# Optimization experiments

Measured on AMD Instinct MI355X. Metric: run time of the kernel, lower is better.

## Reference

```python
import jax, jax.numpy as jnp
import numpy as np

WIN = (2, 7, 7)
DIL = (1, 2, 2)
SHIFT = (1, 3, 3)
HEADS = 3

def _rel_index(win):
    # relative position index, identical to the torch buffer construction
    cs = np.stack(np.meshgrid(np.arange(win[0]), np.arange(win[1]), np.arange(win[2]), indexing='ij'))
    flat = cs.reshape(3, -1)                                  # (3, N)
    rel = (flat[:, :, None] - flat[:, None, :]).transpose(1, 2, 0)  # (N, N, 3)
    rel[..., 0] += win[0] - 1
    rel[..., 1] += win[1] - 1
    rel[..., 2] += win[2] - 1
    rel[..., 1] *= 2 * win[2] - 1
    rel[..., 0] *= (2 * win[1] - 1) * (2 * win[2] - 1)
    return rel.sum(-1)                                        # (N, N) int

REL_IDX = _rel_index(WIN)

def _partition(x, win, dil):
    # x: (B, S, H, W, C) -> (numWin*B, N, C) with dilated window layout
    B, S, H, W, C = x.shape
    x = x.reshape(B, S // (dil[0] * win[0]), dil[0], win[0],
                  H // (dil[1] * win[1]), dil[1], win[1],
                  W // (dil[2] * win[2]), dil[2], win[2], C)
    x = x.transpose(0, 2, 5, 8, 1, 4, 7, 3, 6, 9, 10)
    return x.reshape(-1, win[0] * win[1] * win[2], C)

def _reverse(wins, win, dil, S, H, W, C):
    B = wins.shape[0] * win[0] * win[1] * win[2] // (S * H * W)
    x = wins.reshape(B, dil[0], dil[1], dil[2],
                     S // (dil[0] * win[0]), H // (dil[1] * win[1]), W // (dil[2] * win[2]),
                     win[0], win[1], win[2], C)
    x = x.transpose(0, 4, 1, 7, 5, 2, 8, 6, 3, 9, 10)
    return x.reshape(B, S, H, W, C)

def setup_inputs() -> dict:
    key = jax.random.key(0)
    ks = jax.random.split(key, 4)
    B, S, H, W, C = 4, 8, 112, 112, 96
    tbl = (2 * WIN[0] - 1) * (2 * WIN[1] - 1) * (2 * WIN[2] - 1)
    return {
        'x': jax.random.normal(ks[0], (B, S * H * W, C), jnp.float32),
        'qkv_w': jax.random.normal(ks[1], (3 * C, C), jnp.float32) * 0.02,
        'qkv_b': jnp.zeros((3 * C,), jnp.float32),
        'proj_w': jax.random.normal(ks[2], (C, C), jnp.float32) * 0.02,
        'proj_b': jnp.zeros((C,), jnp.float32),
        'rel_bias_table': jax.random.normal(ks[3], (tbl, HEADS), jnp.float32) * 0.02,
        'S': 8, 'H': 112, 'W': 112,
    }

def reference(x, qkv_w, qkv_b, proj_w, proj_b, rel_bias_table, S, H, W):
    B, L, C = x.shape
    hd = C // HEADS
    scale = hd ** -0.5
    x = x.reshape(B, S, H, W, C)
    true = tuple(w * d for w, d in zip(WIN, DIL))
    tshift = tuple(s * d for s, d in zip(SHIFT, DIL))
    pad_d = (-S) % true[0]; pad_b = (-H) % true[1]; pad_r = (-W) % true[2]
    x = jnp.pad(x, ((0, 0), (0, pad_d), (0, pad_b), (0, pad_r), (0, 0)))
    Sp, Hp, Wp = S + pad_d, H + pad_b, W + pad_r
    if any(s > 0 for s in SHIFT):
        x = jnp.roll(x, (-tshift[0], -tshift[1], -tshift[2]), axis=(1, 2, 3))
    xw = _partition(x, WIN, DIL)                              # (B_, N, C)
    B_, N, _ = xw.shape
    qkv = (xw @ qkv_w.T + qkv_b).reshape(B_, N, 3, HEADS, hd).transpose(2, 0, 3, 1, 4)
    q, k, v = qkv[0] * scale, qkv[1], qkv[2]                  # (B_, h, N, d)
    attn = jnp.einsum('bhnd,bhmd->bhnm', q, k)
    bias = rel_bias_table[REL_IDX.reshape(-1)].reshape(N, N, HEADS).transpose(2, 0, 1)
    attn = jax.nn.softmax(attn + bias[None], axis=-1)
    out = jnp.einsum('bhnm,bhmd->bhnd', attn, v).transpose(0, 2, 1, 3).reshape(B_, N, C)
    out = out @ proj_w.T + proj_b
    x = _reverse(out, WIN, DIL, Sp, Hp, Wp, C)
    if any(s > 0 for s in SHIFT):
        x = jnp.roll(x, tshift, axis=(1, 2, 3))
    x = x[:, :S, :H, :W, :]
    return x.reshape(B, S * H * W, C)
```

## Files before the change

kernel.cpp:

```cpp
#include <hip/hip_runtime.h>
#include <hip/hip_bf16.h>


typedef __attribute__((ext_vector_type(8))) short short8;
typedef __attribute__((ext_vector_type(4))) float f32x4;

#define WQ_ELEMS (288 * 96)
#define WP_ELEMS (96 * 96)
#define BIAS_ELEMS (3 * 112 * 112)
#define LOG2E 1.4426950408889634f

__device__ __forceinline__ unsigned short f2bf(float f) {
  __hip_bfloat16 h = __float2bfloat16(f);
  return *reinterpret_cast<unsigned short*>(&h);
}

__device__ __forceinline__ unsigned int pack_bf2(float a, float b) {
  unsigned int r;
  asm("v_cvt_pk_bf16_f32 %0, %1, %2" : "=v"(r) : "v"(a), "v"(b));
  return r;
}

__device__ __forceinline__ float exp2_hw(float x) {
  float r;
  asm("v_exp_f32 %0, %1" : "=v"(r) : "v"(x));
  return r;
}

__global__ __launch_bounds__(256) void prep_kernel(
    const float* __restrict__ qkv_w, const float* __restrict__ proj_w,
    const float* __restrict__ tbl, unsigned short* __restrict__ wq,
    unsigned short* __restrict__ wp, float* __restrict__ bias) {
  int i = blockIdx.x * 256 + threadIdx.x;
  if (i < WQ_ELEMS) wq[i] = f2bf(qkv_w[i]);
  if (i < WP_ELEMS) wp[i] = f2bf(proj_w[i]);
  if (i < BIAS_ELEMS) {
    int h = i / 12544; int rem = i - h * 12544;
    int m = rem / 112; int n = rem - m * 112;
    float v = -1e30f;
    if (m < 98 && n < 98) {
      int m0 = m / 49, mr = m - m0 * 49, m1 = mr / 7, m2 = mr - m1 * 7;
      int n0 = n / 49, nr = n - n0 * 49, n1 = nr / 7, n2 = nr - n1 * 7;
      int idx = (m0 - n0 + 1) * 169 + (m1 - n1 + 6) * 13 + (m2 - n2 + 6);
      v = tbl[idx * 3 + h] * LOG2E;
    }
    bias[i] = v;
  }
}


__global__ __launch_bounds__(512, 4) void winattn_kernel(
    const float* __restrict__ x, const float* __restrict__ qkv_b,
    const float* __restrict__ proj_b, const unsigned short* __restrict__ wq,
    const unsigned short* __restrict__ wp, const float* __restrict__ bias,
    float* __restrict__ out) {

  __shared__ __align__(16) unsigned short lds[40512];
  __shared__ int eoff[98];

  unsigned short* Qf  = lds;
  unsigned short* Kf  = lds + 9408;
  unsigned short* Vtf = lds + 18816;
  unsigned short* Xf  = lds + 31104;

  const int tid  = threadIdx.x;
  const int wv   = tid >> 6;
  const int lane = tid & 63;
  const int l    = lane & 15;
  const int q    = lane >> 4;

  const short8 zero8 = {0, 0, 0, 0, 0, 0, 0, 0};

  int t1 = blockIdx.x;
  const int wb = t1 & 7;  t1 >>= 3;
  const int hb = t1 & 7;  t1 >>= 3;
  const int sb = t1 & 3;  t1 >>= 2;
  const int d2 = t1 & 1;  t1 >>= 1;
  const int d1 = t1 & 1;  t1 >>= 1;
  const int b  = t1;

  for (int i = tid; i < 768; i += 512)
    reinterpret_cast<unsigned*>(Vtf + 10752)[i] = 0;
  if (tid < 98) {
    int wi0 = tid / 49; int r = tid - wi0 * 49;
    int wi1 = r / 7;    int wi2 = r - wi1 * 7;
    int s  = sb * 2 + wi0;            int so = (s + 1) & 7;
    int hh = (hb * 2 + d1) * 7 + wi1; int ho = hh + 6; if (ho >= 112) ho -= 112;
    int ww = (wb * 2 + d2) * 7 + wi2; int wo = ww + 6; if (wo >= 112) wo -= 112;
    eoff[tid] = (b * 100352 + (so * 112 + ho) * 112 + wo) * 96;
  }
  __syncthreads();

  for (int i = tid; i < 2352; i += 512) {
    int row = i / 24, c4 = i - row * 24;
    float4 v = *reinterpret_cast<const float4*>(x + eoff[row] + c4 * 4);
    uint2 u;
    u.x = pack_bf2(v.x, v.y); u.y = pack_bf2(v.z, v.w);
    *reinterpret_cast<uint2*>(&Xf[((c4 >> 1) * 98 + row) * 8 + (c4 & 1) * 4]) = u;
  }
  __syncthreads();

  const float qscale = 0.17677669529663687f * LOG2E;
  for (int j = wv; j < 19; j += 8) {
    if (j < 12) {
      int ct = j;
      int mch = ct * 16 + l;
      short8 a0 = *reinterpret_cast<const short8*>(wq + mch * 96 +      q * 8);
      short8 a1 = *reinterpret_cast<const short8*>(wq + mch * 96 + 32 + q * 8);
      short8 a2 = *reinterpret_cast<const short8*>(wq + mch * 96 + 64 + q * 8);
      float4 bv = *reinterpret_cast<const float4*>(qkv_b + ct * 16 + q * 4);
      bool isQ = (ct < 6);
      float sc = isQ ? qscale : 1.0f;
      unsigned short* dst = isQ ? Qf : Kf;
      int c0 = (isQ ? ct * 16 : (ct - 6) * 16) + q * 4;
      unsigned short* const dstp = &dst[(c0 >> 3) * 784 + (c0 & 7)];
#pragma unroll
      for (int tt = 0; tt < 7; tt++) {
        int tok = tt * 16 + l;
        short8 b0 = zero8, b1 = zero8, b2 = zero8;
        if (tok < 98) {
          b0 = *reinterpret_cast<const short8*>(&Xf[(( q    ) * 98 + tok) * 8]);
          b1 = *reinterpret_cast<const short8*>(&Xf[((4 + q ) * 98 + tok) * 8]);
          b2 = *reinterpret_cast<const short8*>(&Xf[((8 + q ) * 98 + tok) * 8]);
        }
        f32x4 acc = {0.f, 0.f, 0.f, 0.f};
        acc = __builtin_amdgcn_mfma_f32_16x16x32_bf16(a0, b0, acc, 0, 0, 0);
        acc = __builtin_amdgcn_mfma_f32_16x16x32_bf16(a1, b1, acc, 0, 0, 0);
        acc = __builtin_amdgcn_mfma_f32_16x16x32_bf16(a2, b2, acc, 0, 0, 0);
        uint2 pk;
        pk.x = pack_bf2((acc[0] + bv.x) * sc, (acc[1] + bv.y) * sc);
        pk.y = pack_bf2((acc[2] + bv.z) * sc, (acc[3] + bv.w) * sc);
        if (tok < 98)
          *reinterpret_cast<uint2*>(&dstp[tok * 8]) = pk;
      }
    } else {
      int mt = j - 12;
      int tokf = mt * 16 + l;
      short8 a0 = zero8, a1 = zero8, a2 = zero8;
      if (tokf < 98) {
        a0 = *reinterpret_cast<const short8*>(&Xf[(( q    ) * 98 + tokf) * 8]);
        a1 = *reinterpret_cast<const short8*>(&Xf[((4 + q ) * 98 + tokf) * 8]);
        a2 = *reinterpret_cast<const short8*>(&Xf[((8 + q ) * 98 + tokf) * 8]);
      }
      int tok0 = mt * 16 + q * 4;
#pragma unroll
      for (int vt = 0; vt < 6; vt++) {
        int ch = vt * 16 + l;
        short8 b0 = *reinterpret_cast<const short8*>(wq + (192 + ch) * 96 +      q * 8);
        short8 b1 = *reinterpret_cast<const short8*>(wq + (192 + ch) * 96 + 32 + q * 8);
        short8 b2 = *reinterpret_cast<const short8*>(wq + (192 + ch) * 96 + 64 + q * 8);
        f32x4 acc = {0.f, 0.f, 0.f, 0.f};
        acc = __builtin_amdgcn_mfma_f32_16x16x32_bf16(a0, b0, acc, 0, 0, 0);
        acc = __builtin_amdgcn_mfma_f32_16x16x32_bf16(a1, b1, acc, 0, 0, 0);
        acc = __builtin_amdgcn_mfma_f32_16x16x32_bf16(a2, b2, acc, 0, 0, 0);
        float bvv = qkv_b[192 + ch];
        uint2 pk;
        pk.x = pack_bf2(acc[0] + bvv, acc[1] + bvv);
        pk.y = pack_bf2(acc[2] + bvv, acc[3] + bvv);
        *reinterpret_cast<uint2*>(&Vtf[((tok0 >> 3) * 96 + ch) * 8 + (tok0 & 7)]) = pk;
      }
    }
  }
  __syncthreads();

  unsigned short* PwW = Xf + wv * 1024;
  const int pbase = ((q >> 1) * 16 + l) * 8 + (q & 1) * 4;
  const int rbase = (q * 16 + l) * 8;

  for (int p = wv; p < 21; p += 8) {
    int h = p / 7, mt = p - h * 7;
    int qtok = mt * 16 + l;
    const float* bh = bias + h * 12544 + qtok * 112 + q * 4;
    f32x4 s[7];
#pragma unroll
    for (int nt = 0; nt < 7; nt++) {
      float4 bv = *reinterpret_cast<const float4*>(bh + nt * 16);
      f32x4 a = {bv.x, bv.y, bv.z, bv.w};
      s[nt] = a;
    }
    short8 qa = zero8;
    if (qtok < 98)
      qa = *reinterpret_cast<const short8*>(&Qf[((h * 4 + q) * 98 + qtok) * 8]);
    short8 vf0[4], vf1[4];
#pragma unroll
    for (int kt = 0; kt < 4; kt++) {
      vf0[kt] = *reinterpret_cast<const short8*>(&Vtf[((kt * 4 + q) * 96 + h * 32 + l) * 8]);
      vf1[kt] = *reinterpret_cast<const short8*>(&Vtf[((kt * 4 + q) * 96 + h * 32 + 16 + l) * 8]);
    }
#pragma unroll
    for (int nt = 0; nt < 7; nt++) {
      int key = nt * 16 + l;
      short8 kb = zero8;
      if (key < 98)
        kb = *reinterpret_cast<const short8*>(&Kf[((h * 4 + q) * 98 + key) * 8]);
      s[nt] = __builtin_amdgcn_mfma_f32_16x16x32_bf16(kb, qa, s[nt], 0, 0, 0);
    }
    float t[7];
    uint2 pk[7];
#pragma unroll
    for (int nt = 0; nt < 7; nt++) {
      float e0 = exp2_hw(s[nt][0]);
      float e1 = exp2_hw(s[nt][1]);
      float e2 = exp2_hw(s[nt][2]);
      float e3 = exp2_hw(s[nt][3]);
      t[nt] = (e0 + e1) + (e2 + e3);
      pk[nt].x = pack_bf2(e0, e1);
      pk[nt].y = pack_bf2(e2, e3);
    }
#pragma unroll
    for (int nt = 0; nt < 4; nt++)
      *reinterpret_cast<uint2*>(&PwW[pbase + nt * 256]) = pk[nt];
    float sum = ((t[0] + t[1]) + (t[2] + t[3])) + ((t[4] + t[5]) + t[6]);
    sum += __shfl_xor(sum, 16);
    sum += __shfl_xor(sum, 32);
    float inv = (qtok < 98) ? __builtin_amdgcn_rcpf(sum) : 0.0f;

    f32x4 o0 = {0.f, 0.f, 0.f, 0.f}, o1 = {0.f, 0.f, 0.f, 0.f};
#pragma unroll
    for (int kt = 0; kt < 2; kt++) {
      short8 pa = *reinterpret_cast<const short8*>(&PwW[rbase + kt * 512]);
      o0 = __builtin_amdgcn_mfma_f32_16x16x32_bf16(vf0[kt], pa, o0, 0, 0, 0);
      o1 = __builtin_amdgcn_mfma_f32_16x16x32_bf16(vf1[kt], pa, o1, 0, 0, 0);
    }
    {
      uint2 z; z.x = 0; z.y = 0;
      *reinterpret_cast<uint2*>(&PwW[768 + lane * 4]) = z;
    }
#pragma unroll
    for (int nt = 4; nt < 7; nt++)
      *reinterpret_cast<uint2*>(&PwW[pbase + (nt - 4) * 256]) = pk[nt];
#pragma unroll
    for (int kt = 2; kt < 4; kt++) {
      short8 pa = *reinterpret_cast<const short8*>(&PwW[rbase + (kt - 2) * 512]);
      o0 = __builtin_amdgcn_mfma_f32_16x16x32_bf16(vf0[kt], pa, o0, 0, 0, 0);
      o1 = __builtin_amdgcn_mfma_f32_16x16x32_bf16(vf1[kt], pa, o1, 0, 0, 0);
    }
    if (qtok < 98) {
      int c0 = h * 32 + q * 4;
      uint2 pk0;
      pk0.x = pack_bf2(o0[0] * inv, o0[1] * inv);
      pk0.y = pack_bf2(o0[2] * inv, o0[3] * inv);
      *reinterpret_cast<uint2*>(&Qf[((c0 >> 3) * 98 + qtok) * 8 + (c0 & 7)]) = pk0;
      int c1 = c0 + 16;
      uint2 pk1;
      pk1.x = pack_bf2(o1[0] * inv, o1[1] * inv);
      pk1.y = pack_bf2(o1[2] * inv, o1[3] * inv);
      *reinterpret_cast<uint2*>(&Qf[((c1 >> 3) * 98 + qtok) * 8 + (c1 & 7)]) = pk1;
    }
  }
  __syncthreads();

  for (int t = wv; t < 42; t += 8) {
    int ct = t / 7, tt = t - ct * 7;
    int mch = ct * 16 + l;
    short8 a0 = *reinterpret_cast<const short8*>(wp + mch * 96 +      q * 8);
    short8 a1 = *reinterpret_cast<const short8*>(wp + mch * 96 + 32 + q * 8);
    short8 a2 = *reinterpret_cast<const short8*>(wp + mch * 96 + 64 + q * 8);
    int tok = tt * 16 + l;
    short8 b0 = zero8, b1 = zero8, b2 = zero8;
    if (tok < 98) {
      b0 = *reinterpret_cast<const short8*>(&Qf[(( q    ) * 98 + tok) * 8]);
      b1 = *reinterpret_cast<const short8*>(&Qf[((4 + q ) * 98 + tok) * 8]);
      b2 = *reinterpret_cast<const short8*>(&Qf[((8 + q ) * 98 + tok) * 8]);
    }
    f32x4 acc = {0.f, 0.f, 0.f, 0.f};
    acc = __builtin_amdgcn_mfma_f32_16x16x32_bf16(a0, b0, acc, 0, 0, 0);
    acc = __builtin_amdgcn_mfma_f32_16x16x32_bf16(a1, b1, acc, 0, 0, 0);
    acc = __builtin_amdgcn_mfma_f32_16x16x32_bf16(a2, b2, acc, 0, 0, 0);
    float4 pb = *reinterpret_cast<const float4*>(proj_b + ct * 16 + q * 4);
    if (tok < 98) {
      float4 o;
      o.x = acc[0] + pb.x; o.y = acc[1] + pb.y;
      o.z = acc[2] + pb.z; o.w = acc[3] + pb.w;
      *reinterpret_cast<float4*>(out + eoff[tok] + ct * 16 + q * 4) = o;
    }
  }
}

extern "C" void kernel_launch(void* const* d_in, const int* in_sizes, int n_in,
                              void* d_out, int out_size, void* d_ws, size_t ws_size,
                              hipStream_t stream) {
  const float* x      = (const float*)d_in[0];
  const float* qkv_w  = (const float*)d_in[1];
  const float* qkv_b  = (const float*)d_in[2];
  const float* proj_w = (const float*)d_in[3];
  const float* proj_b = (const float*)d_in[4];
  const float* tbl    = (const float*)d_in[5];

  unsigned short* wq = (unsigned short*)d_ws;
  unsigned short* wp = wq + WQ_ELEMS;
  float* bias = (float*)((char*)d_ws + (WQ_ELEMS + WP_ELEMS) * 2);

  prep_kernel<<<(BIAS_ELEMS + 255) / 256, 256, 0, stream>>>(qkv_w, proj_w, tbl,
                                                            wq, wp, bias);
  winattn_kernel<<<4096, 512, 0, stream>>>(x, qkv_b, proj_b, wq, wp, bias,
                                           (float*)d_out);
}
```

Measured before the change: 395.7 us.

## Raise block size to twelve waves and stream P·V through smaller per-wave buffer

Launches 768 threads (12 waves) per window block instead of 512 and strides all per-wave work loops by 12, so the 21 attention tiles, 19 QKV tiles and 42 projection tiles are spread across more waves. To fit twelve per-wave P scratch areas into the reused X region, each wave's P buffer shrinks to 512 elements, and the P·V product is restructured to write two key tiles at a time and load V fragments per step instead of preloading all eight. This cuts register pressure and LDS footprint per wave but adds more LDS round-trips and leaves some waves idle in loops with uneven tile counts.

```diff
diff --git a/kernel.cpp b/kernel.cpp
--- a/kernel.cpp
+++ b/kernel.cpp
@@ -49,7 +49,7 @@
 }
 
 
-__global__ __launch_bounds__(512, 4) void winattn_kernel(
+__global__ __launch_bounds__(768, 6) void winattn_kernel(
     const float* __restrict__ x, const float* __restrict__ qkv_b,
     const float* __restrict__ proj_b, const unsigned short* __restrict__ wq,
     const unsigned short* __restrict__ wp, const float* __restrict__ bias,
@@ -79,7 +79,7 @@
   const int d1 = t1 & 1;  t1 >>= 1;
   const int b  = t1;
 
-  for (int i = tid; i < 768; i += 512)
+  for (int i = tid; i < 768; i += 768)
     reinterpret_cast<unsigned*>(Vtf + 10752)[i] = 0;
   if (tid < 98) {
     int wi0 = tid / 49; int r = tid - wi0 * 49;
@@ -91,7 +91,7 @@
   }
   __syncthreads();
 
-  for (int i = tid; i < 2352; i += 512) {
+  for (int i = tid; i < 2352; i += 768) {
     int row = i / 24, c4 = i - row * 24;
     float4 v = *reinterpret_cast<const float4*>(x + eoff[row] + c4 * 4);
     uint2 u;
@@ -101,7 +101,7 @@
   __syncthreads();
 
   const float qscale = 0.17677669529663687f * LOG2E;
-  for (int j = wv; j < 19; j += 8) {
+  for (int j = wv; j < 19; j += 12) {
     if (j < 12) {
       int ct = j;
       int mch = ct * 16 + l;
@@ -163,11 +163,11 @@
   }
   __syncthreads();
 
-  unsigned short* PwW = Xf + wv * 1024;
+  unsigned short* PwW = Xf + wv * 512;
   const int pbase = ((q >> 1) * 16 + l) * 8 + (q & 1) * 4;
   const int rbase = (q * 16 + l) * 8;
 
-  for (int p = wv; p < 21; p += 8) {
+  for (int p = wv; p < 21; p += 12) {
     int h = p / 7, mt = p - h * 7;
     int qtok = mt * 16 + l;
     const float* bh = bias + h * 12544 + qtok * 112 + q * 4;
@@ -181,12 +181,6 @@
     short8 qa = zero8;
     if (qtok < 98)
       qa = *reinterpret_cast<const short8*>(&Qf[((h * 4 + q) * 98 + qtok) * 8]);
-    short8 vf0[4], vf1[4];
-#pragma unroll
-    for (int kt = 0; kt < 4; kt++) {
-      vf0[kt] = *reinterpret_cast<const short8*>(&Vtf[((kt * 4 + q) * 96 + h * 32 + l) * 8]);
-      vf1[kt] = *reinterpret_cast<const short8*>(&Vtf[((kt * 4 + q) * 96 + h * 32 + 16 + l) * 8]);
-    }
 #pragma unroll
     for (int nt = 0; nt < 7; nt++) {
       int key = nt * 16 + l;
@@ -207,9 +201,6 @@
       pk[nt].x = pack_bf2(e0, e1);
       pk[nt].y = pack_bf2(e2, e3);
     }
-#pragma unroll
-    for (int nt = 0; nt < 4; nt++)
-      *reinterpret_cast<uint2*>(&PwW[pbase + nt * 256]) = pk[nt];
     float sum = ((t[0] + t[1]) + (t[2] + t[3])) + ((t[4] + t[5]) + t[6]);
     sum += __shfl_xor(sum, 16);
     sum += __shfl_xor(sum, 32);
@@ -217,23 +208,24 @@
 
     f32x4 o0 = {0.f, 0.f, 0.f, 0.f}, o1 = {0.f, 0.f, 0.f, 0.f};
 #pragma unroll
-    for (int kt = 0; kt < 2; kt++) {
-      short8 pa = *reinterpret_cast<const short8*>(&PwW[rbase + kt * 512]);
-      o0 = __builtin_amdgcn_mfma_f32_16x16x32_bf16(vf0[kt], pa, o0, 0, 0, 0);
-      o1 = __builtin_amdgcn_mfma_f32_16x16x32_bf16(vf1[kt], pa, o1, 0, 0, 0);
+    for (int kt = 0; kt < 3; kt++) {
+      *reinterpret_cast<uint2*>(&PwW[pbase])       = pk[2 * kt];
+      *reinterpret_cast<uint2*>(&PwW[pbase + 256]) = pk[2 * kt + 1];
+      short8 v0 = *reinterpret_cast<const short8*>(&Vtf[((kt * 4 + q) * 96 + h * 32 + l) * 8]);
+      short8 v1 = *reinterpret_cast<const short8*>(&Vtf[((kt * 4 + q) * 96 + h * 32 + 16 + l) * 8]);
+      short8 pa = *reinterpret_cast<const short8*>(&PwW[rbase]);
+      o0 = __builtin_amdgcn_mfma_f32_16x16x32_bf16(v0, pa, o0, 0, 0, 0);
+      o1 = __builtin_amdgcn_mfma_f32_16x16x32_bf16(v1, pa, o1, 0, 0, 0);
     }
     {
+      *reinterpret_cast<uint2*>(&PwW[pbase]) = pk[6];
       uint2 z; z.x = 0; z.y = 0;
-      *reinterpret_cast<uint2*>(&PwW[768 + lane * 4]) = z;
-    }
-#pragma unroll
-    for (int nt = 4; nt < 7; nt++)
-      *reinterpret_cast<uint2*>(&PwW[pbase + (nt - 4) * 256]) = pk[nt];
-#pragma unroll
-    for (int kt = 2; kt < 4; kt++) {
-      short8 pa = *reinterpret_cast<const short8*>(&PwW[rbase + (kt - 2) * 512]);
-      o0 = __builtin_amdgcn_mfma_f32_16x16x32_bf16(vf0[kt], pa, o0, 0, 0, 0);
-      o1 = __builtin_amdgcn_mfma_f32_16x16x32_bf16(vf1[kt], pa, o1, 0, 0, 0);
+      *reinterpret_cast<uint2*>(&PwW[256 + lane * 4]) = z;
+      short8 v0 = *reinterpret_cast<const short8*>(&Vtf[((12 + q) * 96 + h * 32 + l) * 8]);
+      short8 v1 = *reinterpret_cast<const short8*>(&Vtf[((12 + q) * 96 + h * 32 + 16 + l) * 8]);
+      short8 pa = *reinterpret_cast<const short8*>(&PwW[rbase]);
+      o0 = __builtin_amdgcn_mfma_f32_16x16x32_bf16(v0, pa, o0, 0, 0, 0);
+      o1 = __builtin_amdgcn_mfma_f32_16x16x32_bf16(v1, pa, o1, 0, 0, 0);
     }
     if (qtok < 98) {
       int c0 = h * 32 + q * 4;
@@ -250,7 +242,7 @@
   }
   __syncthreads();
 
-  for (int t = wv; t < 42; t += 8) {
+  for (int t = wv; t < 42; t += 12) {
     int ct = t / 7, tt = t - ct * 7;
     int mch = ct * 16 + l;
     short8 a0 = *reinterpret_cast<const short8*>(wp + mch * 96 +      q * 8);
@@ -293,6 +285,6 @@
 
   prep_kernel<<<(BIAS_ELEMS + 255) / 256, 256, 0, stream>>>(qkv_w, proj_w, tbl,
                                                             wq, wp, bias);
-  winattn_kernel<<<4096, 512, 0, stream>>>(x, qkv_b, proj_b, wq, wp, bias,
+  winattn_kernel<<<4096, 768, 0, stream>>>(x, qkv_b, proj_b, wq, wp, bias,
                                            (float*)d_out);
 }
```

Result: no change. 388.2 us (-1.9%).
